# Performance work log

Measured on AMD Instinct MI355X. Metric: run time of the kernel, lower is better.

## Reference

```python
import jax, jax.numpy as jnp
import numpy as np

N_NODES = 100000
IN_C = 300
OUT_C = 200
N_EDGES = 1600000
NEG_SLOPE = 0.2  # PyG GATConv default


def setup_inputs() -> dict:
    key = jax.random.key(0)
    ks = jax.random.split(key, 12)
    x = jax.random.normal(ks[0], (N_NODES, IN_C), dtype=jnp.float32)
    edge_index = jax.random.randint(ks[1], (2, N_EDGES), 0, N_NODES, dtype=jnp.int64)
    s0 = 1.0 / np.sqrt(IN_C)
    s1 = 1.0 / np.sqrt(OUT_C)
    return {
        "x": x,
        "W0": jax.random.normal(ks[2], (IN_C, OUT_C), dtype=jnp.float32) * s0,
        "a_src0": jax.random.normal(ks[3], (OUT_C,), dtype=jnp.float32) * s1,
        "a_dst0": jax.random.normal(ks[4], (OUT_C,), dtype=jnp.float32) * s1,
        "b0": jnp.zeros((OUT_C,), dtype=jnp.float32),
        "W1": jax.random.normal(ks[5], (OUT_C, OUT_C), dtype=jnp.float32) * s1,
        "a_src1": jax.random.normal(ks[6], (OUT_C,), dtype=jnp.float32) * s1,
        "a_dst1": jax.random.normal(ks[7], (OUT_C,), dtype=jnp.float32) * s1,
        "b1": jnp.zeros((OUT_C,), dtype=jnp.float32),
        "edge_index": edge_index,
    }


def _gat_conv(x, W, a_src, a_dst, b, src, dst, n):
    # h: [N, F'] projected features
    h = x @ W
    alpha_src = h @ a_src  # [N]
    alpha_dst = h @ a_dst  # [N]
    # per-edge raw attention score, message flows src -> dst
    e = jax.nn.leaky_relu(alpha_src[src] + alpha_dst[dst], NEG_SLOPE)  # [E]
    # segment softmax over incoming edges of each destination node
    m = jax.ops.segment_max(e, dst, num_segments=n)
    ex = jnp.exp(e - m[dst])
    denom = jax.ops.segment_sum(ex, dst, num_segments=n)
    alpha = ex / denom[dst]  # [E]
    # scatter-add weighted messages
    out = jax.ops.segment_sum(h[src] * alpha[:, None], dst, num_segments=n)
    return out + b


def reference(x, W0, a_src0, a_dst0, b0, W1, a_src1, a_dst1, b1, edge_index):
    n = x.shape[0]
    # PyG GATConv default: add self-loops
    loops = jnp.arange(n, dtype=edge_index.dtype)
    src = jnp.concatenate([edge_index[0], loops])
    dst = jnp.concatenate([edge_index[1], loops])
    h = jax.nn.relu(_gat_conv(x, W0, a_src0, a_dst0, b0, src, dst, n))
    h = jax.nn.relu(_gat_conv(h, W1, a_src1, a_dst1, b1, src, dst, n))
    return h
```

## Files before the change

kernel.cpp:

```cpp
#include <hip/hip_runtime.h>

#define IN_C 300
#define OUT_C 200
#define NEG_SLOPE 0.2f

#define BMB 64
#define BMW 16
#define BKC 20
#define WF4 1000

static inline int cdiv(long a, int b) { return (int)((a + b - 1) / b); }

__device__ __forceinline__ void glds16(const float* g, float* l) {
  __builtin_amdgcn_global_load_lds(
      (const __attribute__((address_space(1))) void*)g,
      (__attribute__((address_space(3))) void*)l, 16, 0, 0);
}

__global__ __launch_bounds__(256)
void zero_int_kernel(int* __restrict__ p, int n) {
  int i = blockIdx.x * blockDim.x + threadIdx.x;
  if (i < n) p[i] = 0;
}

__device__ __forceinline__ void edge_sd(const int* __restrict__ src,
                                        const int* __restrict__ dst,
                                        int i, int E, int& s, int& d) {
  if (i < E) { s = src[i]; d = dst[i]; } else { s = d = i - E; }
}

__global__ __launch_bounds__(256)
void hist_kernel(const int* __restrict__ src, const int* __restrict__ dst,
                 int E, int ET, int* __restrict__ counts) {
  int i = blockIdx.x * blockDim.x + threadIdx.x;
  if (i >= ET) return;
  int s, d; edge_sd(src, dst, i, E, s, d);
  atomicAdd(counts + d, 1);
}

__global__ __launch_bounds__(256)
void scan_a_kernel(const int* __restrict__ in, int n, int* __restrict__ out,
                   int* __restrict__ bsums) {
  __shared__ int lds[256];
  int t = threadIdx.x;
  int base = blockIdx.x * 1024 + t * 4;
  int v0 = (base + 0 < n) ? in[base + 0] : 0;
  int v1 = (base + 1 < n) ? in[base + 1] : 0;
  int v2 = (base + 2 < n) ? in[base + 2] : 0;
  int v3 = (base + 3 < n) ? in[base + 3] : 0;
  int s1 = v0 + v1, s2 = s1 + v2, s3 = s2 + v3;
  lds[t] = s3;
  __syncthreads();
  for (int o = 1; o < 256; o <<= 1) {
    int x = (t >= o) ? lds[t - o] : 0;
    __syncthreads();
    lds[t] += x;
    __syncthreads();
  }
  int pre = (t > 0) ? lds[t - 1] : 0;
  if (base + 0 < n) out[base + 0] = pre + v0;
  if (base + 1 < n) out[base + 1] = pre + s1;
  if (base + 2 < n) out[base + 2] = pre + s2;
  if (base + 3 < n) out[base + 3] = pre + s3;
  if (t == 255) bsums[blockIdx.x] = lds[255];
}

__global__ __launch_bounds__(256)
void scan_b_kernel(int* __restrict__ bs, int nb) {
  __shared__ int lds[256];
  int t = threadIdx.x;
  lds[t] = (t < nb) ? bs[t] : 0;
  __syncthreads();
  for (int o = 1; o < 256; o <<= 1) {
    int x = (t >= o) ? lds[t - o] : 0;
    __syncthreads();
    lds[t] += x;
    __syncthreads();
  }
  if (t < nb) bs[t] = lds[t];
}

__global__ __launch_bounds__(256)
void scan_c_kernel(int* __restrict__ out, int n, const int* __restrict__ bs) {
  int i = blockIdx.x * blockDim.x + threadIdx.x;
  if (i >= n) return;
  int b = i >> 10;
  if (b > 0) out[i] += bs[b - 1];
}

__global__ __launch_bounds__(256)
void fill_kernel(const int* __restrict__ src, const int* __restrict__ dst,
                 int E, int ET, const int* __restrict__ rowptr,
                 int* __restrict__ cursor, int* __restrict__ csr_src) {
  int i = blockIdx.x * blockDim.x + threadIdx.x;
  if (i >= ET) return;
  int s, d; edge_sd(src, dst, i, E, s, d);
  int pos = rowptr[d] + atomicAdd(cursor + d, 1);
  csr_src[pos] = s;
}

__global__ __launch_bounds__(256)
void gemm_ws_kernel(const float* __restrict__ A, const float* __restrict__ W,
                    const float* __restrict__ a_src, const float* __restrict__ a_dst,
                    float* __restrict__ H, float* __restrict__ asN,
                    float* __restrict__ adN, int K, int N) {
  __shared__ float Wf[4096];
  __shared__ float As[2][BMB][BKC];
  int t = threadIdx.x;
  int wave = t >> 6, lane = t & 63;
  int col = lane * 4;
  long row0 = (long)blockIdx.x * BMB;
  int wrow = wave * BMW;

  const bool pw3ok = t < (WF4 - 768);
  float4 pw0, pw1, pw2, pw3;
  const float* wsrc = W;
  auto loadW = [&]() {
    pw0 = *(const float4*)(wsrc + t * 4);
    pw1 = *(const float4*)(wsrc + 1024 + t * 4);
    pw2 = *(const float4*)(wsrc + 2048 + t * 4);
    if (pw3ok) pw3 = *(const float4*)(wsrc + 3072 + t * 4);
    wsrc += BKC * OUT_C;
  };
  auto writeW = [&]() {
    float4* wf4 = (float4*)Wf;
    wf4[t] = pw0; wf4[256 + t] = pw1; wf4[512 + t] = pw2;
    if (pw3ok) wf4[768 + t] = pw3;
  };

  int f0 = t;
  long ar0 = row0 + f0 / 5; if (ar0 >= N) ar0 = N - 1;
  const float* sA0 = A + ar0 * K + (f0 % 5) * 4;
  int f1 = 256 + t;
  long ar1 = row0 + f1 / 5; if (ar1 >= N) ar1 = N - 1;
  const float* sA1 = A + ar1 * K + (f1 % 5) * 4;
  auto loadA = [&](int buf) {
    glds16(sA0, (float*)As[buf] + wave * 256);
    if (t < 64) glds16(sA1, (float*)As[buf] + 1024);
    sA0 += BKC; sA1 += BKC;
  };

  float4 acc[BMW];
  #pragma unroll
  for (int r = 0; r < BMW; ++r) acc[r] = make_float4(0.f, 0.f, 0.f, 0.f);

  const int nch = K / BKC;
  loadW();
  loadA(0);
  int cur = 0;
  for (int ch = 0; ch < nch; ++ch) {
    __syncthreads();
    writeW();
    __syncthreads();
    if (ch + 1 < nch) { loadW(); loadA(cur ^ 1); }
    #pragma unroll
    for (int kk = 0; kk < BKC; kk += 4) {
      float4 w0 = *(float4*)&Wf[(kk + 0) * OUT_C + col];
      float4 w1 = *(float4*)&Wf[(kk + 1) * OUT_C + col];
      float4 w2 = *(float4*)&Wf[(kk + 2) * OUT_C + col];
      float4 w3 = *(float4*)&Wf[(kk + 3) * OUT_C + col];
      #pragma unroll
      for (int r = 0; r < BMW; ++r) {
        float4 a = *(float4*)&As[cur][wrow + r][kk];
        acc[r].x = fmaf(a.x, w0.x, acc[r].x);
        acc[r].x = fmaf(a.y, w1.x, acc[r].x);
        acc[r].x = fmaf(a.z, w2.x, acc[r].x);
        acc[r].x = fmaf(a.w, w3.x, acc[r].x);
        acc[r].y = fmaf(a.x, w0.y, acc[r].y);
        acc[r].y = fmaf(a.y, w1.y, acc[r].y);
        acc[r].y = fmaf(a.z, w2.y, acc[r].y);
        acc[r].y = fmaf(a.w, w3.y, acc[r].y);
        acc[r].z = fmaf(a.x, w0.z, acc[r].z);
        acc[r].z = fmaf(a.y, w1.z, acc[r].z);
        acc[r].z = fmaf(a.z, w2.z, acc[r].z);
        acc[r].z = fmaf(a.w, w3.z, acc[r].z);
        acc[r].w = fmaf(a.x, w0.w, acc[r].w);
        acc[r].w = fmaf(a.y, w1.w, acc[r].w);
        acc[r].w = fmaf(a.z, w2.w, acc[r].w);
        acc[r].w = fmaf(a.w, w3.w, acc[r].w);
      }
    }
    cur ^= 1;
  }

  bool cok = col < OUT_C;
  #pragma unroll
  for (int r = 0; r < BMW; ++r) {
    long grow = row0 + wrow + r;
    if (cok && grow < N) *(float4*)(H + grow * OUT_C + col) = acc[r];
  }
  float4 vs = make_float4(0.f, 0.f, 0.f, 0.f);
  float4 vd = make_float4(0.f, 0.f, 0.f, 0.f);
  if (cok) {
    vs = *(const float4*)(a_src + col);
    vd = *(const float4*)(a_dst + col);
  }
  #pragma unroll
  for (int r = 0; r < BMW; ++r) {
    float ss = acc[r].x * vs.x + acc[r].y * vs.y + acc[r].z * vs.z + acc[r].w * vs.w;
    float sd = acc[r].x * vd.x + acc[r].y * vd.y + acc[r].z * vd.z + acc[r].w * vd.w;
    #pragma unroll
    for (int o = 32; o > 0; o >>= 1) {
      ss += __shfl_xor(ss, o);
      sd += __shfl_xor(sd, o);
    }
    long grow = row0 + wrow + r;
    if (lane == 0 && grow < N) { asN[grow] = ss; adN[grow] = sd; }
  }
}

__global__ __launch_bounds__(256)
void gather_agg_kernel(const float* __restrict__ h, const float* __restrict__ asN,
                       const float* __restrict__ adN, const int* __restrict__ rowptr,
                       const int* __restrict__ csr_src, const float* __restrict__ bias,
                       float* __restrict__ out, int N) {
  int wid = (int)(((long)blockIdx.x * blockDim.x + threadIdx.x) >> 6);
  int lane = threadIdx.x & 63;
  if (wid >= N) return;
  int start = rowptr[wid], end = rowptr[wid + 1];
  float ad = adN[wid];
  int c = lane * 4;
  bool cok = c < OUT_C;
  const float* hc = h + c;

  float4 acc = make_float4(0.f, 0.f, 0.f, 0.f);
  float se = 0.f;
  int j = start;
  for (; j + 4 <= end; j += 4) {
    int s0 = csr_src[j], s1 = csr_src[j + 1];
    int s2 = csr_src[j + 2], s3 = csr_src[j + 3];
    float e0 = asN[s0] + ad, e1 = asN[s1] + ad;
    float e2 = asN[s2] + ad, e3 = asN[s3] + ad;
    e0 = e0 > 0.f ? e0 : NEG_SLOPE * e0;
    e1 = e1 > 0.f ? e1 : NEG_SLOPE * e1;
    e2 = e2 > 0.f ? e2 : NEG_SLOPE * e2;
    e3 = e3 > 0.f ? e3 : NEG_SLOPE * e3;
    float w0 = __expf(e0), w1 = __expf(e1), w2 = __expf(e2), w3 = __expf(e3);
    se += (w0 + w1) + (w2 + w3);
    if (cok) {
      float4 h0 = *(const float4*)(hc + (long)s0 * OUT_C);
      float4 h1 = *(const float4*)(hc + (long)s1 * OUT_C);
      float4 h2 = *(const float4*)(hc + (long)s2 * OUT_C);
      float4 h3 = *(const float4*)(hc + (long)s3 * OUT_C);
      acc.x = fmaf(w0, h0.x, acc.x); acc.x = fmaf(w1, h1.x, acc.x);
      acc.x = fmaf(w2, h2.x, acc.x); acc.x = fmaf(w3, h3.x, acc.x);
      acc.y = fmaf(w0, h0.y, acc.y); acc.y = fmaf(w1, h1.y, acc.y);
      acc.y = fmaf(w2, h2.y, acc.y); acc.y = fmaf(w3, h3.y, acc.y);
      acc.z = fmaf(w0, h0.z, acc.z); acc.z = fmaf(w1, h1.z, acc.z);
      acc.z = fmaf(w2, h2.z, acc.z); acc.z = fmaf(w3, h3.z, acc.z);
      acc.w = fmaf(w0, h0.w, acc.w); acc.w = fmaf(w1, h1.w, acc.w);
      acc.w = fmaf(w2, h2.w, acc.w); acc.w = fmaf(w3, h3.w, acc.w);
    }
  }
  for (; j < end; ++j) {
    int s0 = csr_src[j];
    float e0 = asN[s0] + ad;
    e0 = e0 > 0.f ? e0 : NEG_SLOPE * e0;
    float w0 = __expf(e0);
    se += w0;
    if (cok) {
      float4 h0 = *(const float4*)(hc + (long)s0 * OUT_C);
      acc.x = fmaf(w0, h0.x, acc.x);
      acc.y = fmaf(w0, h0.y, acc.y);
      acc.z = fmaf(w0, h0.z, acc.z);
      acc.w = fmaf(w0, h0.w, acc.w);
    }
  }
  if (cok) {
    float inv = 1.0f / se;
    float4 bv = *(const float4*)(bias + c);
    float4 o;
    o.x = fmaxf(fmaf(acc.x, inv, bv.x), 0.f);
    o.y = fmaxf(fmaf(acc.y, inv, bv.y), 0.f);
    o.z = fmaxf(fmaf(acc.z, inv, bv.z), 0.f);
    o.w = fmaxf(fmaf(acc.w, inv, bv.w), 0.f);
    *(float4*)(out + (long)wid * OUT_C + c) = o;
  }
}

static void run_layer(const float* xin, int K, const float* W,
                      const float* a_s, const float* a_d, const float* b,
                      const int* rowptr, const int* csr_src, int N,
                      float* hbuf, float* asN, float* adN, float* outbuf,
                      hipStream_t stream) {
  gemm_ws_kernel<<<cdiv(N, BMB), 256, 0, stream>>>(xin, W, a_s, a_d,
                                                   hbuf, asN, adN, K, N);
  gather_agg_kernel<<<cdiv((long)N * 64, 256), 256, 0, stream>>>(
      hbuf, asN, adN, rowptr, csr_src, b, outbuf, N);
}

extern "C" void kernel_launch(void* const* d_in, const int* in_sizes, int n_in,
                              void* d_out, int out_size, void* d_ws, size_t ws_size,
                              hipStream_t stream) {
  const float* x   = (const float*)d_in[0];
  const float* W0  = (const float*)d_in[1];
  const float* as0 = (const float*)d_in[2];
  const float* ad0 = (const float*)d_in[3];
  const float* b0  = (const float*)d_in[4];
  const float* W1  = (const float*)d_in[5];
  const float* as1 = (const float*)d_in[6];
  const float* ad1 = (const float*)d_in[7];
  const float* b1  = (const float*)d_in[8];
  const int*   ei  = (const int*)d_in[9];

  const int N  = in_sizes[0] / IN_C;
  const int E  = in_sizes[9] / 2;
  const int ET = E + N;
  const int* src = ei;
  const int* dst = ei + E;

  float* out = (float*)d_out;

  char* ws = (char*)d_ws;
  float* hbuf   = (float*)ws;
  float* asN    = (float*)(ws + (size_t)N * OUT_C * 4);
  float* adN    = asN + N;
  int*   rowptr = (int*)(adN + N);
  int*   counts = rowptr + (N + 1);
  int*   bsums  = counts + N;
  int*   csrsrc = bsums + 256;

  const int nb = cdiv(N, 1024);

  zero_int_kernel<<<cdiv(N, 256), 256, 0, stream>>>(counts, N);
  hist_kernel<<<cdiv(ET, 256), 256, 0, stream>>>(src, dst, E, ET, counts);
  scan_a_kernel<<<nb, 256, 0, stream>>>(counts, N, rowptr + 1, bsums);
  scan_b_kernel<<<1, 256, 0, stream>>>(bsums, nb);
  scan_c_kernel<<<cdiv(N, 256), 256, 0, stream>>>(rowptr + 1, N, bsums);
  zero_int_kernel<<<1, 256, 0, stream>>>(rowptr, 1);
  zero_int_kernel<<<cdiv(N, 256), 256, 0, stream>>>(counts, N);
  fill_kernel<<<cdiv(ET, 256), 256, 0, stream>>>(src, dst, E, ET, rowptr, counts, csrsrc);

  run_layer(x, IN_C, W0, as0, ad0, b0, rowptr, csrsrc, N, hbuf, asN, adN, out, stream);
  run_layer(out, OUT_C, W1, as1, ad1, b1, rowptr, csrsrc, N, hbuf, asN, adN, out, stream);
}
```

Measured before the change: 1.116 ms.

## Load GEMM A tile into registers and broadcast via readlane instead of LDS

The GEMM kernel no longer stages the A tile in shared memory through global_load_lds. Each lane now loads strided A elements into registers, and the values are broadcast to the wave with readlane while the FMAs run. The chunk loop is unrolled by two, ping-ponging between two register buffers. This removes the LDS traffic for A, but adds many scalar readlane operations and uncoalesced 4-byte global loads, which could end up costing more than the LDS reads they replace.

```diff
diff --git a/kernel.cpp b/kernel.cpp
--- a/kernel.cpp
+++ b/kernel.cpp
@@ -11,10 +11,8 @@
 
 static inline int cdiv(long a, int b) { return (int)((a + b - 1) / b); }
 
-__device__ __forceinline__ void glds16(const float* g, float* l) {
-  __builtin_amdgcn_global_load_lds(
-      (const __attribute__((address_space(1))) void*)g,
-      (__attribute__((address_space(3))) void*)l, 16, 0, 0);
+__device__ __forceinline__ float rdlane(float v, int l) {
+  return __int_as_float(__builtin_amdgcn_readlane(__float_as_int(v), l));
 }
 
 __global__ __launch_bounds__(256)
@@ -105,7 +103,6 @@
                     float* __restrict__ H, float* __restrict__ asN,
                     float* __restrict__ adN, int K, int N) {
   __shared__ float Wf[4096];
-  __shared__ float As[2][BMB][BKC];
   int t = threadIdx.x;
   int wave = t >> 6, lane = t & 63;
   int col = lane * 4;
@@ -128,59 +125,68 @@
     if (pw3ok) wf4[768 + t] = pw3;
   };
 
-  int f0 = t;
-  long ar0 = row0 + f0 / 5; if (ar0 >= N) ar0 = N - 1;
-  const float* sA0 = A + ar0 * K + (f0 % 5) * 4;
-  int f1 = 256 + t;
-  long ar1 = row0 + f1 / 5; if (ar1 >= N) ar1 = N - 1;
-  const float* sA1 = A + ar1 * K + (f1 % 5) * 4;
-  auto loadA = [&](int buf) {
-    glds16(sA0, (float*)As[buf] + wave * 256);
-    if (t < 64) glds16(sA1, (float*)As[buf] + 1024);
-    sA0 += BKC; sA1 += BKC;
+  long arow = row0 + wrow + (lane >> 2);
+  if (arow >= N) arow = N - 1;
+  const float* abase = A + arow * K + (lane & 3);
+  float plA[5], plB[5];
+  auto loadA = [&](float (&pl)[5]) {
+    #pragma unroll
+    for (int p = 0; p < 5; ++p) pl[p] = abase[p * 4];
+    abase += BKC;
   };
 
   float4 acc[BMW];
   #pragma unroll
   for (int r = 0; r < BMW; ++r) acc[r] = make_float4(0.f, 0.f, 0.f, 0.f);
 
+  auto compute = [&](const float (&pl)[5]) {
+    #pragma unroll
+    for (int p = 0; p < 5; ++p) {
+      float4 w0 = *(float4*)&Wf[(p * 4 + 0) * OUT_C + col];
+      float4 w1 = *(float4*)&Wf[(p * 4 + 1) * OUT_C + col];
+      float4 w2 = *(float4*)&Wf[(p * 4 + 2) * OUT_C + col];
+      float4 w3 = *(float4*)&Wf[(p * 4 + 3) * OUT_C + col];
+      #pragma unroll
+      for (int r = 0; r < BMW; ++r) {
+        float a0 = rdlane(pl[p], r * 4 + 0);
+        float a1 = rdlane(pl[p], r * 4 + 1);
+        float a2 = rdlane(pl[p], r * 4 + 2);
+        float a3 = rdlane(pl[p], r * 4 + 3);
+        acc[r].x = fmaf(a0, w0.x, acc[r].x);
+        acc[r].x = fmaf(a1, w1.x, acc[r].x);
+        acc[r].x = fmaf(a2, w2.x, acc[r].x);
+        acc[r].x = fmaf(a3, w3.x, acc[r].x);
+        acc[r].y = fmaf(a0, w0.y, acc[r].y);
+        acc[r].y = fmaf(a1, w1.y, acc[r].y);
+        acc[r].y = fmaf(a2, w2.y, acc[r].y);
+        acc[r].y = fmaf(a3, w3.y, acc[r].y);
+        acc[r].z = fmaf(a0, w0.z, acc[r].z);
+        acc[r].z = fmaf(a1, w1.z, acc[r].z);
+        acc[r].z = fmaf(a2, w2.z, acc[r].z);
+        acc[r].z = fmaf(a3, w3.z, acc[r].z);
+        acc[r].w = fmaf(a0, w0.w, acc[r].w);
+        acc[r].w = fmaf(a1, w1.w, acc[r].w);
+        acc[r].w = fmaf(a2, w2.w, acc[r].w);
+        acc[r].w = fmaf(a3, w3.w, acc[r].w);
+      }
+    }
+  };
+
   const int nch = K / BKC;
   loadW();
-  loadA(0);
-  int cur = 0;
-  for (int ch = 0; ch < nch; ++ch) {
+  loadA(plA);
+  for (int ch = 0; ch < nch; ch += 2) {
     __syncthreads();
     writeW();
     __syncthreads();
-    if (ch + 1 < nch) { loadW(); loadA(cur ^ 1); }
-    #pragma unroll
-    for (int kk = 0; kk < BKC; kk += 4) {
-      float4 w0 = *(float4*)&Wf[(kk + 0) * OUT_C + col];
-      float4 w1 = *(float4*)&Wf[(kk + 1) * OUT_C + col];
-      float4 w2 = *(float4*)&Wf[(kk + 2) * OUT_C + col];
-      float4 w3 = *(float4*)&Wf[(kk + 3) * OUT_C + col];
-      #pragma unroll
-      for (int r = 0; r < BMW; ++r) {
-        float4 a = *(float4*)&As[cur][wrow + r][kk];
-        acc[r].x = fmaf(a.x, w0.x, acc[r].x);
-        acc[r].x = fmaf(a.y, w1.x, acc[r].x);
-        acc[r].x = fmaf(a.z, w2.x, acc[r].x);
-        acc[r].x = fmaf(a.w, w3.x, acc[r].x);
-        acc[r].y = fmaf(a.x, w0.y, acc[r].y);
-        acc[r].y = fmaf(a.y, w1.y, acc[r].y);
-        acc[r].y = fmaf(a.z, w2.y, acc[r].y);
-        acc[r].y = fmaf(a.w, w3.y, acc[r].y);
-        acc[r].z = fmaf(a.x, w0.z, acc[r].z);
-        acc[r].z = fmaf(a.y, w1.z, acc[r].z);
-        acc[r].z = fmaf(a.z, w2.z, acc[r].z);
-        acc[r].z = fmaf(a.w, w3.z, acc[r].z);
-        acc[r].w = fmaf(a.x, w0.w, acc[r].w);
-        acc[r].w = fmaf(a.y, w1.w, acc[r].w);
-        acc[r].w = fmaf(a.z, w2.w, acc[r].w);
-        acc[r].w = fmaf(a.w, w3.w, acc[r].w);
-      }
-    }
-    cur ^= 1;
+    if (ch + 1 < nch) { loadW(); loadA(plB); }
+    compute(plA);
+    if (ch + 1 >= nch) break;
+    __syncthreads();
+    writeW();
+    __syncthreads();
+    if (ch + 2 < nch) { loadW(); loadA(plA); }
+    compute(plB);
   }
 
   bool cok = col < OUT_C;
```

New measurement: 1.136 ms. No clear change (+1.8%).
